# Performance work log

Hardware: AMD Instinct MI355X
Metric: run time of the kernel (lower is better)

## Reference

```python
import jax, jax.numpy as jnp
import numpy as np

SYNC = 0.15
DEBATE = 0.15
N_FACTIONS = 8


def faction_sync_debate(h, step):
    # h: [Na, H] hidden rows of alive cells (contiguous, as gathered by alive_idx)
    n, H = h.shape
    n_f = min(N_FACTIONS, n // 2)
    if n_f < 2:
        return h
    fs = n // n_f
    hb = h[: n_f * fs].reshape(n_f, fs, H)
    fm = hb.mean(axis=1, keepdims=True)                  # faction means
    hb = (1.0 - SYNC) * hb + SYNC * fm                   # sync toward faction mean
    if step > 5:                                          # step is a static Python int
        # post-sync faction means equal pre-sync means; global opinion = mean of faction means
        go = hb.mean(axis=1).mean(axis=0)                # [H]
        dc = max(1, fs // 4)
        hb = hb.at[:, :dc].set((1.0 - DEBATE) * hb[:, :dc] + DEBATE * go)
    return jnp.concatenate([hb.reshape(n_f * fs, H), h[n_f * fs:]], axis=0)


def setup_inputs() -> dict:
    key = jax.random.key(0)
    ks = jax.random.split(key, 16)
    n_cells, n_alive = 262144, 131072
    in_d, hid, out_d = 64, 128, 64
    s = 0.1
    alive_idx = jnp.sort(jax.random.permutation(ks[14], n_cells)[:n_alive])
    return {
        "x": jax.random.normal(ks[0], (1, in_d), jnp.float32),
        "hiddens": jax.random.normal(ks[1], (n_cells, hid), jnp.float32) * 0.1,
        "Wa1": jax.random.normal(ks[2], (128, in_d + hid), jnp.float32) * s,
        "ba1": jax.random.normal(ks[3], (128,), jnp.float32) * s,
        "Wa2": jax.random.normal(ks[4], (out_d, 128), jnp.float32) * s,
        "ba2": jax.random.normal(ks[5], (out_d,), jnp.float32) * s,
        "Wg1": jax.random.normal(ks[6], (128, in_d + hid), jnp.float32) * s,
        "bg1": jax.random.normal(ks[7], (128,), jnp.float32) * s,
        "Wg2": jax.random.normal(ks[8], (out_d, 128), jnp.float32) * s,
        "bg2": jax.random.normal(ks[9], (out_d,), jnp.float32) * s,
        "W_ih": jax.random.normal(ks[10], (3 * hid, out_d + 1), jnp.float32) * s,
        "W_hh": jax.random.normal(ks[11], (3 * hid, hid), jnp.float32) * s,
        "b_ih": jax.random.normal(ks[12], (3 * hid,), jnp.float32) * s,
        "b_hh": jax.random.normal(ks[13], (3 * hid,), jnp.float32) * s,
        "alive_idx": alive_idx,
        "step": 10,
    }


def reference(x, hiddens, Wa1, ba1, Wa2, ba2, Wg1, bg1, Wg2, bg2,
              W_ih, W_hh, b_ih, b_hh, alive_idx, step):
    # Gather alive cells and run the tiny MLP+GRU for all of them at once
    h = hiddens[alive_idx]                                # [Na, H]
    xb = jnp.broadcast_to(x, (h.shape[0], x.shape[-1]))   # same x for every cell
    c = jnp.concatenate([xb, h], axis=-1)                 # [Na, in+H]
    a = jax.nn.relu(c @ Wa1.T + ba1) @ Wa2.T + ba2        # engine_a
    g = jax.nn.relu(c @ Wg1.T + bg1) @ Wg2.T + bg2        # engine_g
    out = a - g                                           # [Na, D]
    tension = jnp.mean(out * out, axis=-1, keepdims=True) # [Na, 1]
    # GRUCell (torch gate order r, z, n); mem_input is detached in the original
    mem_in = jax.lax.stop_gradient(jnp.concatenate([out, tension], axis=-1))
    gi = mem_in @ W_ih.T + b_ih                           # [Na, 3H]
    gh = h @ W_hh.T + b_hh                                # [Na, 3H]
    H = h.shape[-1]
    ir, iz, inn = gi[:, :H], gi[:, H:2 * H], gi[:, 2 * H:]
    hr, hz, hn = gh[:, :H], gh[:, H:2 * H], gh[:, 2 * H:]
    r = jax.nn.sigmoid(ir + hr)
    z = jax.nn.sigmoid(iz + hz)
    nn_ = jnp.tanh(inn + r * hn)
    new_h = jax.lax.stop_gradient((1.0 - z) * nn_ + z * h)  # detached in original
    new_h = faction_sync_debate(new_h, step)
    new_hiddens = hiddens.at[alive_idx].set(new_h)        # scatter-back state update
    # tension-softmax-weighted combination (weights detached via .item() in torch)
    t = tension[:, 0]
    w = jax.lax.stop_gradient(jax.nn.softmax(t, axis=0))
    combined = jnp.sum(w[:, None] * out, axis=0, keepdims=True)  # [1, D]
    mean_tension = jnp.mean(jax.lax.stop_gradient(t))
    return combined, mean_tension, new_hiddens
```

## Files before the change

### kernel.cpp

```cpp
#include <hip/hip_runtime.h>
#include <math.h>

#define TMC 64

typedef __attribute__((ext_vector_type(4))) float f32x4;
typedef __attribute__((ext_vector_type(8))) short bf16x8;

#define MFMA16(a,b,c) __builtin_amdgcn_mfma_f32_16x16x32_bf16((a),(b),(c),0,0,0)

__device__ __forceinline__ float sigmoidf_(float x){ return 1.0f/(1.0f + __expf(-x)); }
__device__ __forceinline__ float tanhf_(float x){
  float e = __expf(2.0f*x);
  return 1.0f - 2.0f/(e + 1.0f);
}

__device__ __forceinline__ unsigned short f2bf(float f){
  unsigned u = __float_as_uint(f);
  unsigned r = (u + 0x7FFFu + ((u>>16)&1u)) >> 16;
  return (unsigned short)r;
}
__device__ __forceinline__ unsigned pack2(float a, float b){
  return (unsigned)f2bf(a) | ((unsigned)f2bf(b)<<16);
}
__device__ __forceinline__ float bf2f(unsigned short u){ return __uint_as_float(((unsigned)u)<<16); }

__device__ __forceinline__ bf16x8 lds_ld8(const ushort* base, int byte){
  return *reinterpret_cast<const bf16x8*>(reinterpret_cast<const char*>(base) + byte);
}

__global__ void k_pre(const float* __restrict__ x,
                      const float* __restrict__ Wa1, const float* __restrict__ ba1,
                      const float* __restrict__ Wg1, const float* __restrict__ bg1,
                      const float* __restrict__ ba2, const float* __restrict__ bg2,
                      const float* __restrict__ bih, const float* __restrict__ bhh,
                      float* __restrict__ xab, float* __restrict__ b2d, float* __restrict__ brz){
  __shared__ float sx[64];
  int tid = threadIdx.x;
  if (tid < 64) sx[tid] = x[tid];
  __syncthreads();
  if (tid < 128){
    const float* w = Wa1 + tid*192;
    float s = ba1[tid];
    #pragma unroll
    for (int i=0;i<64;i++) s += w[i]*sx[i];
    xab[tid] = s;
  } else {
    int j = tid-128;
    const float* w = Wg1 + j*192;
    float s = bg1[j];
    #pragma unroll
    for (int i=0;i<64;i++) s += w[i]*sx[i];
    xab[tid] = s;
  }
  if (tid < 64) b2d[tid] = ba2[tid] - bg2[tid];
  brz[tid] = bih[tid] + bhh[tid];
}

__global__ void k_pack(const float* __restrict__ Wa1, const float* __restrict__ Wg1,
                       const float* __restrict__ Wa2, const float* __restrict__ Wg2,
                       const float* __restrict__ Wih, const float* __restrict__ Whh,
                       ushort* __restrict__ W1f, ushort* __restrict__ W2f,
                       ushort* __restrict__ Wgf, ushort* __restrict__ Whf,
                       float* __restrict__ w64){
  int stride = gridDim.x*blockDim.x;
  int t0 = blockIdx.x*blockDim.x + threadIdx.x;
  for (int i=t0; i<256*128; i+=stride){
    int e=i&7, lane=(i>>3)&63, ks=(i>>9)&3, nt=i>>11;
    int r = nt*16 + (lane&15), k = ks*32 + (lane>>4)*8 + e;
    float v = (r<128) ? Wa1[r*192+64+k] : Wg1[(r-128)*192+64+k];
    W1f[i] = f2bf(v);
  }
  for (int i=t0; i<128*128; i+=stride){
    int e=i&7, lane=(i>>3)&63, ks=(i>>9)&3, nt=i>>11;
    int r = nt*16 + (lane&15), k = ks*32 + (lane>>4)*8 + e;
    float v = (r<64) ? Wa2[r*128+k] : Wg2[(r-64)*128+k];
    W2f[i] = f2bf(v);
  }
  for (int i=t0; i<384*64; i+=stride){
    int e=i&7, lane=(i>>3)&63, ks=(i>>9)&1, nt=i>>10;
    int r = nt*16 + (lane&15), k = ks*32 + (lane>>4)*8 + e;
    Wgf[i] = f2bf(Wih[r*65+k]);
  }
  for (int i=t0; i<384*128; i+=stride){
    int e=i&7, lane=(i>>3)&63, ks=(i>>9)&3, nt=i>>11;
    int r = nt*16 + (lane&15), k = ks*32 + (lane>>4)*8 + e;
    Whf[i] = f2bf(Whh[r*128+k]);
  }
  for (int i=t0; i<384; i+=stride) w64[i] = Wih[i*65+64];
}

__global__ void k_mark(const int* __restrict__ alive, int* __restrict__ iflags, int n){
  int i = blockIdx.x*blockDim.x + threadIdx.x;
  if (i < n) iflags[alive[i]] = i + 1;
}

__global__ __launch_bounds__(256,2) void k_main(
    const float* __restrict__ hiddens, const int* __restrict__ alive,
    const ushort* __restrict__ W1f, const ushort* __restrict__ W2f,
    const ushort* __restrict__ Wgf, const ushort* __restrict__ Whf,
    const float* __restrict__ w64,
    const float* __restrict__ xab, const float* __restrict__ b2d,
    const float* __restrict__ brz,
    const float* __restrict__ bih, const float* __restrict__ bhh,
    float* __restrict__ nh, float* __restrict__ facsum,
    float* __restrict__ recs, unsigned* __restrict__ tmax_u, float* __restrict__ tsum,
    int n, int fs, int nffs)
{
  __shared__ ushort sH[64*128];
  __shared__ __align__(16) ushort arena[64*256];
  __shared__ float sTS[4][64];
  __shared__ float sT[64];
  __shared__ float sE[64];
  __shared__ int   sIdx[TMC];

  ushort* sV1  = arena;
  ushort* sMIH = arena;

  int tid = threadIdx.x;
  int lane = tid & 63;
  int w = tid >> 6;
  int l15 = lane & 15;
  int lg  = lane >> 4;

  int base = blockIdx.x * TMC;
  int nvalid = n - base; if (nvalid > TMC) nvalid = TMC;

  if (tid < TMC){
    int t2 = tid < nvalid ? tid : (nvalid-1);
    sIdx[tid] = alive[base + t2];
  }
  __syncthreads();

  {
    int m = tid >> 2, c0 = (tid & 3) * 32;
    const float* src = hiddens + (size_t)sIdx[m]*128 + c0;
    #pragma unroll
    for (int j=0; j<32; j+=8){
      float4 v0 = *(const float4*)(src + j);
      float4 v1 = *(const float4*)(src + j + 4);
      uint4 pk;
      pk.x = pack2(v0.x, v0.y); pk.y = pack2(v0.z, v0.w);
      pk.z = pack2(v1.x, v1.y); pk.w = pack2(v1.z, v1.w);
      int byte = (m*256 + (c0 + j)*2) ^ ((m&7)<<4);
      *reinterpret_cast<uint4*>(reinterpret_cast<char*>(sH) + byte) = pk;
    }
  }
  __syncthreads();

  {
    int c0 = w*64;
    f32x4 acc[4][4];
    #pragma unroll
    for (int tm=0;tm<4;tm++)
      #pragma unroll
      for (int tn=0;tn<4;tn++) acc[tm][tn] = (f32x4)0.f;
    #pragma unroll
    for (int ks=0; ks<4; ks++){
      bf16x8 a[4], b[4];
      #pragma unroll
      for (int tm=0;tm<4;tm++){
        int row = tm*16 + l15;
        a[tm] = lds_ld8(sH, (row*256 + ks*64 + lg*16) ^ ((row&7)<<4));
      }
      #pragma unroll
      for (int tn=0;tn<4;tn++)
        b[tn] = *(const bf16x8*)(W1f + ((((w*4+tn)*4 + ks)*64 + lane)<<3));
      #pragma unroll
      for (int tm=0;tm<4;tm++)
        #pragma unroll
        for (int tn=0;tn<4;tn++)
          acc[tm][tn] = MFMA16(a[tm], b[tn], acc[tm][tn]);
    }
    #pragma unroll
    for (int tn=0;tn<4;tn++){
      int col = c0 + tn*16 + l15;
      float bias = xab[col];
      #pragma unroll
      for (int tm=0;tm<4;tm++){
        #pragma unroll
        for (int r=0;r<4;r++){
          int row = tm*16 + lg*4 + r;
          float v = fmaxf(acc[tm][tn][r] + bias, 0.f);
          int byte = (row*512 + col*2) ^ ((row&7)<<4);
          *(ushort*)((char*)sV1 + byte) = f2bf(v);
        }
      }
    }
  }
  __syncthreads();

  int jo2 = w*16;
  float outv[4][4];
  {
    f32x4 accA[4], accG[4];
    #pragma unroll
    for (int tm=0;tm<4;tm++){ accA[tm]=(f32x4)0.f; accG[tm]=(f32x4)0.f; }
    #pragma unroll
    for (int ks=0; ks<4; ks++){
      bf16x8 aA[4], aG[4], bA, bG;
      #pragma unroll
      for (int tm=0;tm<4;tm++){
        int row = tm*16 + l15;
        aA[tm] = lds_ld8(sV1, (row*512 + ks*64 + lg*16) ^ ((row&7)<<4));
        aG[tm] = lds_ld8(sV1, (row*512 + 256 + ks*64 + lg*16) ^ ((row&7)<<4));
      }
      bA = *(const bf16x8*)(W2f + (((w*4 + ks)*64 + lane)<<3));
      bG = *(const bf16x8*)(W2f + ((((4+w)*4 + ks)*64 + lane)<<3));
      #pragma unroll
      for (int tm=0;tm<4;tm++){
        accA[tm] = MFMA16(aA[tm], bA, accA[tm]);
        accG[tm] = MFMA16(aG[tm], bG, accG[tm]);
      }
    }
    int col = jo2 + l15;
    float bias = b2d[col];
    #pragma unroll
    for (int tm=0;tm<4;tm++)
      #pragma unroll
      for (int r=0;r<4;r++)
        outv[tm][r] = accA[tm][r] - accG[tm][r] + bias;
  }
  __syncthreads();

  {
    int col = jo2 + l15;
    float p[4][4];
    #pragma unroll
    for (int tm=0;tm<4;tm++){
      #pragma unroll
      for (int r=0;r<4;r++){
        int row = tm*16 + lg*4 + r;
        float o = outv[tm][r];
        int byte = (row*128 + col*2) ^ ((row&7)<<4);
        *(ushort*)((char*)sMIH + byte) = f2bf(o);
        p[tm][r] = o*o;
      }
    }
    #pragma unroll
    for (int off=1; off<16; off<<=1)
      #pragma unroll
      for (int tm=0;tm<4;tm++)
        #pragma unroll
        for (int r=0;r<4;r++) p[tm][r] += __shfl_xor(p[tm][r], off);
    if (l15 == 0){
      #pragma unroll
      for (int tm=0;tm<4;tm++)
        #pragma unroll
        for (int r=0;r<4;r++) sTS[w][tm*16 + lg*4 + r] = p[tm][r];
    }
  }
  __syncthreads();

  if (w == 0){
    int row = lane;
    float t = (sTS[0][row] + sTS[1][row] + sTS[2][row] + sTS[3][row]) * (1.0f/64.0f);
    sT[row] = t;
    bool valid = row < nvalid;
    float m2 = valid ? t : -1.f;
    #pragma unroll
    for (int off=1; off<64; off<<=1) m2 = fmaxf(m2, __shfl_xor(m2, off));
    float e  = valid ? __expf(t - m2) : 0.f;
    float st = valid ? t : 0.f;
    float se = e, ss = st;
    #pragma unroll
    for (int off=1; off<64; off<<=1){ se += __shfl_xor(se, off); ss += __shfl_xor(ss, off); }
    sE[row] = e;
    if (lane == 0){
      float* rec = recs + (size_t)blockIdx.x*66;
      rec[0] = m2; rec[1] = se;
      atomicMax(tmax_u, __float_as_uint(m2));
      atomicAdd(tsum, ss);
    }
  }
  __syncthreads();

  {
    float np = 0.f;
    #pragma unroll
    for (int tm=0;tm<4;tm++)
      #pragma unroll
      for (int r=0;r<4;r++)
        np += sE[tm*16 + lg*4 + r] * outv[tm][r];
    np += __shfl_xor(np, 16);
    np += __shfl_xor(np, 32);
    if (lg == 0) recs[(size_t)blockIdx.x*66 + 2 + jo2 + l15] = np;
  }

  int lastrow = nvalid;
  if (base + lastrow > nffs) lastrow = nffs - base;
  int f0 = (fs > 0 && base < nffs) ? base / fs : 0;
  bool onefac = (lastrow <= 0) || ((base + lastrow - 1) / fs == f0);

  {
    int jo3 = w*32;
    int ntb = 2*w;
    f32x4 aR[4][2], aZ[4][2], aN[4][2], aI[4][2];
    #pragma unroll
    for (int tm=0;tm<4;tm++)
      #pragma unroll
      for (int tn=0;tn<2;tn++){
        aR[tm][tn]=(f32x4)0.f; aZ[tm][tn]=(f32x4)0.f;
        aN[tm][tn]=(f32x4)0.f; aI[tm][tn]=(f32x4)0.f;
      }

    #pragma unroll
    for (int ks=0; ks<4; ks++){
      bf16x8 a[4];
      #pragma unroll
      for (int tm=0;tm<4;tm++){
        int row = tm*16 + l15;
        a[tm] = lds_ld8(sH, (row*256 + ks*64 + lg*16) ^ ((row&7)<<4));
      }
      bf16x8 bR[2], bZ[2], bN[2];
      #pragma unroll
      for (int tn=0;tn<2;tn++){
        bR[tn] = *(const bf16x8*)(Whf + ((((     ntb+tn)*4 + ks)*64 + lane)<<3));
        bZ[tn] = *(const bf16x8*)(Whf + ((((8  + ntb+tn)*4 + ks)*64 + lane)<<3));
        bN[tn] = *(const bf16x8*)(Whf + ((((16 + ntb+tn)*4 + ks)*64 + lane)<<3));
      }
      #pragma unroll
      for (int tm=0;tm<4;tm++)
        #pragma unroll
        for (int tn=0;tn<2;tn++){
          aR[tm][tn] = MFMA16(a[tm], bR[tn], aR[tm][tn]);
          aZ[tm][tn] = MFMA16(a[tm], bZ[tn], aZ[tm][tn]);
          aN[tm][tn] = MFMA16(a[tm], bN[tn], aN[tm][tn]);
        }
    }
    #pragma unroll
    for (int ks=0; ks<2; ks++){
      bf16x8 a[4];
      #pragma unroll
      for (int tm=0;tm<4;tm++){
        int row = tm*16 + l15;
        a[tm] = lds_ld8(sMIH, (row*128 + ks*64 + lg*16) ^ ((row&7)<<4));
      }
      bf16x8 bR[2], bZ[2], bI[2];
      #pragma unroll
      for (int tn=0;tn<2;tn++){
        bR[tn] = *(const bf16x8*)(Wgf + ((((     ntb+tn)*2 + ks)*64 + lane)<<3));
        bZ[tn] = *(const bf16x8*)(Wgf + ((((8  + ntb+tn)*2 + ks)*64 + lane)<<3));
        bI[tn] = *(const bf16x8*)(Wgf + ((((16 + ntb+tn)*2 + ks)*64 + lane)<<3));
      }
      #pragma unroll
      for (int tm=0;tm<4;tm++)
        #pragma unroll
        for (int tn=0;tn<2;tn++){
          aR[tm][tn] = MFMA16(a[tm], bR[tn], aR[tm][tn]);
          aZ[tm][tn] = MFMA16(a[tm], bZ[tn], aZ[tm][tn]);
          aI[tm][tn] = MFMA16(a[tm], bI[tn], aI[tm][tn]);
        }
    }

    #pragma unroll
    for (int tn=0;tn<2;tn++){
      int col = jo3 + tn*16 + l15;
      float bR0 = brz[col],      wR = w64[col];
      float bZ0 = brz[128+col],  wZ = w64[128+col];
      float bI0 = bih[256+col],  wI = w64[256+col];
      float bN0 = bhh[256+col];
      float fsum = 0.f;
      #pragma unroll
      for (int tm=0;tm<4;tm++){
        #pragma unroll
        for (int r=0;r<4;r++){
          int row = tm*16 + lg*4 + r;
          float t = sT[row];
          float rr = sigmoidf_(aR[tm][tn][r] + bR0 + t*wR);
          float zz = sigmoidf_(aZ[tm][tn][r] + bZ0 + t*wZ);
          float nnv = tanhf_(aI[tm][tn][r] + bI0 + t*wI + rr*(aN[tm][tn][r] + bN0));
          int hb = (row*256 + col*2) ^ ((row&7)<<4);
          float hv = bf2f(*(const ushort*)((const char*)sH + hb));
          float v = (1.f - zz)*nnv + zz*hv;
          if (row < nvalid) nh[(size_t)sIdx[row]*128 + col] = v;
          if (onefac){
            if (row < lastrow) fsum += v;
          } else if (row < lastrow){
            atomicAdd(&facsum[((base+row)/fs)*128 + col], v);
          }
        }
      }
      if (onefac && lastrow > 0){
        fsum += __shfl_xor(fsum, 16);
        fsum += __shfl_xor(fsum, 32);
        if (lg == 0) atomicAdd(&facsum[f0*128 + col], fsum);
      }
    }
  }
}

__global__ void k_comb1(const float* __restrict__ recs, int nrec,
                        const unsigned* __restrict__ tmax_u,
                        float* __restrict__ num, float* __restrict__ S){
  int tid = threadIdx.x;
  int c = tid & 63, rg = tid >> 6;
  float M = __uint_as_float(*tmax_u);
  float acc = 0.f, sacc = 0.f;
  for (int r = blockIdx.x*4 + rg; r < nrec; r += gridDim.x*4){
    const float* rec = recs + (size_t)r*66;
    float e = __expf(rec[0] - M);
    acc += e * rec[2+c];
    if (c == 0) sacc += e * rec[1];
  }
  __shared__ float sn[4][64];
  __shared__ float ss[4];
  sn[rg][c] = acc;
  if (c == 0) ss[rg] = sacc;
  __syncthreads();
  if (tid < 64) atomicAdd(&num[tid], sn[0][tid]+sn[1][tid]+sn[2][tid]+sn[3][tid]);
  if (tid == 64) atomicAdd(S, ss[0]+ss[1]+ss[2]+ss[3]);
}

__global__ void k_final(const float* __restrict__ num, const float* __restrict__ S,
                        const float* __restrict__ tsum, const float* __restrict__ facsum,
                        float* __restrict__ out, float* __restrict__ go, float* __restrict__ fmn,
                        int n, int n_f, int fs){
  int tid = threadIdx.x;
  if (tid < 64) out[tid] = num[tid] / *S;
  else if (tid == 64) out[64] = *tsum / (float)n;
  if (tid >= 128 && n_f >= 2){
    int j = tid - 128;
    float s = 0.f;
    for (int f=0; f<n_f; f++){
      float v = facsum[f*128+j];
      s += v;
      fmn[f*128+j] = v / (float)fs;
    }
    go[j] = s / (float)(n_f*fs);
  }
}

__global__ void k_post(const float* __restrict__ hid, const int* __restrict__ iflags,
                       const float* __restrict__ fmn, const float* __restrict__ go,
                       const int* __restrict__ step_p,
                       float* __restrict__ nh, int fs, int dc, int nffs, int total){
  bool debate = (*step_p > 5);
  int stride = gridDim.x*blockDim.x;
  for (int idx = blockIdx.x*blockDim.x + threadIdx.x; idx < total; idx += stride){
    int c = idx >> 5, q = idx & 31, j0 = q*4;
    size_t off = (size_t)c*128 + j0;
    int fl = iflags[c];
    if (fl == 0){
      float4 h4 = *(const float4*)(hid + off);
      nh[off] = h4.x; nh[off+1] = h4.y; nh[off+2] = h4.z; nh[off+3] = h4.w;
    } else {
      int i = fl - 1;
      if (i < nffs){
        float v0 = nh[off], v1 = nh[off+1], v2 = nh[off+2], v3 = nh[off+3];
        int f = i / fs;
        float4 fm4 = *(const float4*)(fmn + f*128 + j0);
        v0 = 0.85f*v0 + 0.15f*fm4.x;
        v1 = 0.85f*v1 + 0.15f*fm4.y;
        v2 = 0.85f*v2 + 0.15f*fm4.z;
        v3 = 0.85f*v3 + 0.15f*fm4.w;
        if (debate && (i - f*fs) < dc){
          float4 g4 = *(const float4*)(go + j0);
          v0 = 0.85f*v0 + 0.15f*g4.x;
          v1 = 0.85f*v1 + 0.15f*g4.y;
          v2 = 0.85f*v2 + 0.15f*g4.z;
          v3 = 0.85f*v3 + 0.15f*g4.w;
        }
        nh[off] = v0; nh[off+1] = v1; nh[off+2] = v2; nh[off+3] = v3;
      }
    }
  }
}

extern "C" void kernel_launch(void* const* d_in, const int* in_sizes, int n_in,
                              void* d_out, int out_size, void* d_ws, size_t ws_size,
                              hipStream_t stream){
  const float* x    = (const float*)d_in[0];
  const float* hid  = (const float*)d_in[1];
  const float* Wa1  = (const float*)d_in[2];
  const float* ba1  = (const float*)d_in[3];
  const float* Wa2  = (const float*)d_in[4];
  const float* ba2  = (const float*)d_in[5];
  const float* Wg1  = (const float*)d_in[6];
  const float* bg1  = (const float*)d_in[7];
  const float* Wg2  = (const float*)d_in[8];
  const float* bg2  = (const float*)d_in[9];
  const float* Wih  = (const float*)d_in[10];
  const float* Whh  = (const float*)d_in[11];
  const float* bih  = (const float*)d_in[12];
  const float* bhh  = (const float*)d_in[13];
  const int*   alive= (const int*)d_in[14];
  const int*   step = (const int*)d_in[15];

  int n = in_sizes[14];
  int n_cells = in_sizes[1] / 128;
  int n_f = (n/2 < 8) ? n/2 : 8;
  int fs   = (n_f >= 2) ? n / n_f : 0;
  int nffs = (n_f >= 2) ? n_f * fs : 0;
  int dc   = (fs/4 > 1) ? fs/4 : 1;
  int nblocks = (n + TMC - 1) / TMC;

  float* out = (float*)d_out;
  float* nh  = out + 65;
  float* ws  = (float*)d_ws;

  float* xab   = ws + 0;
  float* b2d   = ws + 256;
  float* brz   = ws + 320;
  float* facs  = ws + 576;
  float* num   = ws + 1600;
  float* Ssum  = ws + 1664;
  float* tsum  = ws + 1665;
  unsigned* tmax_u = (unsigned*)(ws + 1666);
  float* go    = ws + 1668;
  float* fmn   = ws + 1796;
  float* w64   = ws + 2820;
  float* recs  = ws + 3204;
  int recs_end = 3204 + ((nblocks*66 + 3) & ~3);
  int* iflags  = (int*)(ws + recs_end);
  int woff = (recs_end + n_cells + 3) & ~3;
  ushort* W1f  = (ushort*)(ws + woff);
  ushort* W2f  = (ushort*)(ws + woff + 16384);
  ushort* Wgf  = (ushort*)(ws + woff + 24576);
  ushort* Whf  = (ushort*)(ws + woff + 36864);

  hipMemsetAsync(ws + 576, 0, 1092*sizeof(float), stream);
  hipMemsetAsync(iflags, 0, (size_t)n_cells*sizeof(int), stream);

  k_pre<<<1,256,0,stream>>>(x, Wa1, ba1, Wg1, bg1, ba2, bg2, bih, bhh, xab, b2d, brz);
  k_pack<<<256,256,0,stream>>>(Wa1, Wg1, Wa2, Wg2, Wih, Whh, W1f, W2f, Wgf, Whf, w64);
  k_mark<<<(n+255)/256,256,0,stream>>>(alive, iflags, n);
  k_main<<<nblocks,256,0,stream>>>(hid, alive, W1f, W2f, Wgf, Whf, w64, xab, b2d, brz,
                                   bih, bhh, nh, facs, recs, tmax_u, tsum,
                                   n, fs, nffs);
  k_comb1<<<64,256,0,stream>>>(recs, nblocks, tmax_u, num, Ssum);
  k_final<<<1,256,0,stream>>>(num, Ssum, tsum, facs, out, go, fmn, n, n_f, fs);
  k_post<<<2048,256,0,stream>>>(hid, iflags, fmn, go, step, nh, fs, dc, nffs, n_cells*32);
}
```

Baseline: 183.4 us.

## Split k_main work across 8 waves with 512-thread blocks

```diff
diff --git a/kernel.cpp b/kernel.cpp
--- a/kernel.cpp
+++ b/kernel.cpp
@@ -94,7 +94,7 @@
   if (i < n) iflags[alive[i]] = i + 1;
 }
 
-__global__ __launch_bounds__(256,2) void k_main(
+__global__ __launch_bounds__(512,4) void k_main(
     const float* __restrict__ hiddens, const int* __restrict__ alive,
     const ushort* __restrict__ W1f, const ushort* __restrict__ W2f,
     const ushort* __restrict__ Wgf, const ushort* __restrict__ Whf,
@@ -108,7 +108,8 @@
 {
   __shared__ ushort sH[64*128];
   __shared__ __align__(16) ushort arena[64*256];
-  __shared__ float sTS[4][64];
+  __shared__ float sTS[8][32];
+  __shared__ float sNp[2][64];
   __shared__ float sT[64];
   __shared__ float sE[64];
   __shared__ int   sIdx[TMC];
@@ -132,10 +133,10 @@
   __syncthreads();
 
   {
-    int m = tid >> 2, c0 = (tid & 3) * 32;
+    int m = tid >> 3, c0 = (tid & 7) * 16;
     const float* src = hiddens + (size_t)sIdx[m]*128 + c0;
     #pragma unroll
-    for (int j=0; j<32; j+=8){
+    for (int j=0; j<16; j+=8){
       float4 v0 = *(const float4*)(src + j);
       float4 v1 = *(const float4*)(src + j + 4);
       uint4 pk;
@@ -148,32 +149,29 @@
   __syncthreads();
 
   {
-    int c0 = w*64;
-    f32x4 acc[4][4];
-    #pragma unroll
-    for (int tm=0;tm<4;tm++)
-      #pragma unroll
-      for (int tn=0;tn<4;tn++) acc[tm][tn] = (f32x4)0.f;
+    f32x4 acc[4][2];
+    #pragma unroll
+    for (int tm=0;tm<4;tm++){ acc[tm][0]=(f32x4)0.f; acc[tm][1]=(f32x4)0.f; }
     #pragma unroll
     for (int ks=0; ks<4; ks++){
-      bf16x8 a[4], b[4];
+      bf16x8 a[4], b[2];
       #pragma unroll
       for (int tm=0;tm<4;tm++){
         int row = tm*16 + l15;
         a[tm] = lds_ld8(sH, (row*256 + ks*64 + lg*16) ^ ((row&7)<<4));
       }
       #pragma unroll
-      for (int tn=0;tn<4;tn++)
-        b[tn] = *(const bf16x8*)(W1f + ((((w*4+tn)*4 + ks)*64 + lane)<<3));
+      for (int tn=0;tn<2;tn++)
+        b[tn] = *(const bf16x8*)(W1f + ((((w*2+tn)*4 + ks)*64 + lane)<<3));
       #pragma unroll
       for (int tm=0;tm<4;tm++)
         #pragma unroll
-        for (int tn=0;tn<4;tn++)
+        for (int tn=0;tn<2;tn++)
           acc[tm][tn] = MFMA16(a[tm], b[tn], acc[tm][tn]);
     }
     #pragma unroll
-    for (int tn=0;tn<4;tn++){
-      int col = c0 + tn*16 + l15;
+    for (int tn=0;tn<2;tn++){
+      int col = (w*2+tn)*16 + l15;
       float bias = xab[col];
       #pragma unroll
       for (int tm=0;tm<4;tm++){
@@ -189,25 +187,26 @@
   }
   __syncthreads();
 
-  int jo2 = w*16;
-  float outv[4][4];
+  int ct = w & 3, mh = w >> 2;
+  int jo2 = ct*16;
+  float outv[2][4];
   {
-    f32x4 accA[4], accG[4];
-    #pragma unroll
-    for (int tm=0;tm<4;tm++){ accA[tm]=(f32x4)0.f; accG[tm]=(f32x4)0.f; }
+    f32x4 accA[2], accG[2];
+    #pragma unroll
+    for (int tm=0;tm<2;tm++){ accA[tm]=(f32x4)0.f; accG[tm]=(f32x4)0.f; }
     #pragma unroll
     for (int ks=0; ks<4; ks++){
-      bf16x8 aA[4], aG[4], bA, bG;
-      #pragma unroll
-      for (int tm=0;tm<4;tm++){
-        int row = tm*16 + l15;
+      bf16x8 aA[2], aG[2], bA, bG;
+      #pragma unroll
+      for (int tm=0;tm<2;tm++){
+        int row = mh*32 + tm*16 + l15;
         aA[tm] = lds_ld8(sV1, (row*512 + ks*64 + lg*16) ^ ((row&7)<<4));
         aG[tm] = lds_ld8(sV1, (row*512 + 256 + ks*64 + lg*16) ^ ((row&7)<<4));
       }
-      bA = *(const bf16x8*)(W2f + (((w*4 + ks)*64 + lane)<<3));
-      bG = *(const bf16x8*)(W2f + ((((4+w)*4 + ks)*64 + lane)<<3));
-      #pragma unroll
-      for (int tm=0;tm<4;tm++){
+      bA = *(const bf16x8*)(W2f + (((ct*4 + ks)*64 + lane)<<3));
+      bG = *(const bf16x8*)(W2f + ((((4+ct)*4 + ks)*64 + lane)<<3));
+      #pragma unroll
+      for (int tm=0;tm<2;tm++){
         accA[tm] = MFMA16(aA[tm], bA, accA[tm]);
         accG[tm] = MFMA16(aG[tm], bG, accG[tm]);
       }
@@ -215,7 +214,7 @@
     int col = jo2 + l15;
     float bias = b2d[col];
     #pragma unroll
-    for (int tm=0;tm<4;tm++)
+    for (int tm=0;tm<2;tm++)
       #pragma unroll
       for (int r=0;r<4;r++)
         outv[tm][r] = accA[tm][r] - accG[tm][r] + bias;
@@ -224,12 +223,12 @@
 
   {
     int col = jo2 + l15;
-    float p[4][4];
-    #pragma unroll
-    for (int tm=0;tm<4;tm++){
+    float p[2][4];
+    #pragma unroll
+    for (int tm=0;tm<2;tm++){
       #pragma unroll
       for (int r=0;r<4;r++){
-        int row = tm*16 + lg*4 + r;
+        int row = mh*32 + tm*16 + lg*4 + r;
         float o = outv[tm][r];
         int byte = (row*128 + col*2) ^ ((row&7)<<4);
         *(ushort*)((char*)sMIH + byte) = f2bf(o);
@@ -239,12 +238,12 @@
     #pragma unroll
     for (int off=1; off<16; off<<=1)
       #pragma unroll
-      for (int tm=0;tm<4;tm++)
+      for (int tm=0;tm<2;tm++)
         #pragma unroll
         for (int r=0;r<4;r++) p[tm][r] += __shfl_xor(p[tm][r], off);
     if (l15 == 0){
       #pragma unroll
-      for (int tm=0;tm<4;tm++)
+      for (int tm=0;tm<2;tm++)
         #pragma unroll
         for (int r=0;r<4;r++) sTS[w][tm*16 + lg*4 + r] = p[tm][r];
     }
@@ -253,7 +252,8 @@
 
   if (w == 0){
     int row = lane;
-    float t = (sTS[0][row] + sTS[1][row] + sTS[2][row] + sTS[3][row]) * (1.0f/64.0f);
+    int hh = row >> 5, ri = row & 31;
+    float t = (sTS[hh*4+0][ri] + sTS[hh*4+1][ri] + sTS[hh*4+2][ri] + sTS[hh*4+3][ri]) * (1.0f/64.0f);
     sT[row] = t;
     bool valid = row < nvalid;
     float m2 = valid ? t : -1.f;
@@ -277,14 +277,16 @@
   {
     float np = 0.f;
     #pragma unroll
-    for (int tm=0;tm<4;tm++)
+    for (int tm=0;tm<2;tm++)
       #pragma unroll
       for (int r=0;r<4;r++)
-        np += sE[tm*16 + lg*4 + r] * outv[tm][r];
+        np += sE[mh*32 + tm*16 + lg*4 + r] * outv[tm][r];
     np += __shfl_xor(np, 16);
     np += __shfl_xor(np, 32);
-    if (lg == 0) recs[(size_t)blockIdx.x*66 + 2 + jo2 + l15] = np;
-  }
+    if (lg == 0) sNp[mh][jo2 + l15] = np;
+  }
+  __syncthreads();
+  if (tid < 64) recs[(size_t)blockIdx.x*66 + 2 + tid] = sNp[0][tid] + sNp[1][tid];
 
   int lastrow = nvalid;
   if (base + lastrow > nffs) lastrow = nffs - base;
@@ -292,16 +294,11 @@
   bool onefac = (lastrow <= 0) || ((base + lastrow - 1) / fs == f0);
 
   {
-    int jo3 = w*32;
-    int ntb = 2*w;
-    f32x4 aR[4][2], aZ[4][2], aN[4][2], aI[4][2];
-    #pragma unroll
-    for (int tm=0;tm<4;tm++)
-      #pragma unroll
-      for (int tn=0;tn<2;tn++){
-        aR[tm][tn]=(f32x4)0.f; aZ[tm][tn]=(f32x4)0.f;
-        aN[tm][tn]=(f32x4)0.f; aI[tm][tn]=(f32x4)0.f;
-      }
+    f32x4 aR[4], aZ[4], aN[4], aI[4];
+    #pragma unroll
+    for (int tm=0;tm<4;tm++){
+      aR[tm]=(f32x4)0.f; aZ[tm]=(f32x4)0.f; aN[tm]=(f32x4)0.f; aI[tm]=(f32x4)0.f;
+    }
 
     #pragma unroll
     for (int ks=0; ks<4; ks++){
@@ -311,21 +308,15 @@
         int row = tm*16 + l15;
         a[tm] = lds_ld8(sH, (row*256 + ks*64 + lg*16) ^ ((row&7)<<4));
       }
-      bf16x8 bR[2], bZ[2], bN[2];
-      #pragma unroll
-      for (int tn=0;tn<2;tn++){
-        bR[tn] = *(const bf16x8*)(Whf + ((((     ntb+tn)*4 + ks)*64 + lane)<<3));
-        bZ[tn] = *(const bf16x8*)(Whf + ((((8  + ntb+tn)*4 + ks)*64 + lane)<<3));
-        bN[tn] = *(const bf16x8*)(Whf + ((((16 + ntb+tn)*4 + ks)*64 + lane)<<3));
-      }
-      #pragma unroll
-      for (int tm=0;tm<4;tm++)
-        #pragma unroll
-        for (int tn=0;tn<2;tn++){
-          aR[tm][tn] = MFMA16(a[tm], bR[tn], aR[tm][tn]);
-          aZ[tm][tn] = MFMA16(a[tm], bZ[tn], aZ[tm][tn]);
-          aN[tm][tn] = MFMA16(a[tm], bN[tn], aN[tm][tn]);
-        }
+      bf16x8 bR = *(const bf16x8*)(Whf + (((      w *4 + ks)*64 + lane)<<3));
+      bf16x8 bZ = *(const bf16x8*)(Whf + ((((8  + w)*4 + ks)*64 + lane)<<3));
+      bf16x8 bN = *(const bf16x8*)(Whf + ((((16 + w)*4 + ks)*64 + lane)<<3));
+      #pragma unroll
+      for (int tm=0;tm<4;tm++){
+        aR[tm] = MFMA16(a[tm], bR, aR[tm]);
+        aZ[tm] = MFMA16(a[tm], bZ, aZ[tm]);
+        aN[tm] = MFMA16(a[tm], bN, aN[tm]);
+      }
     }
     #pragma unroll
     for (int ks=0; ks<2; ks++){
@@ -335,26 +326,19 @@
         int row = tm*16 + l15;
         a[tm] = lds_ld8(sMIH, (row*128 + ks*64 + lg*16) ^ ((row&7)<<4));
       }
-      bf16x8 bR[2], bZ[2], bI[2];
-      #pragma unroll
-      for (int tn=0;tn<2;tn++){
-        bR[tn] = *(const bf16x8*)(Wgf + ((((     ntb+tn)*2 + ks)*64 + lane)<<3));
-        bZ[tn] = *(const bf16x8*)(Wgf + ((((8  + ntb+tn)*2 + ks)*64 + lane)<<3));
-        bI[tn] = *(const bf16x8*)(Wgf + ((((16 + ntb+tn)*2 + ks)*64 + lane)<<3));
-      }
-      #pragma unroll
-      for (int tm=0;tm<4;tm++)
-        #pragma unroll
-        for (int tn=0;tn<2;tn++){
-          aR[tm][tn] = MFMA16(a[tm], bR[tn], aR[tm][tn]);
-          aZ[tm][tn] = MFMA16(a[tm], bZ[tn], aZ[tm][tn]);
-          aI[tm][tn] = MFMA16(a[tm], bI[tn], aI[tm][tn]);
-        }
-    }
-
-    #pragma unroll
-    for (int tn=0;tn<2;tn++){
-      int col = jo3 + tn*16 + l15;
+      bf16x8 bR = *(const bf16x8*)(Wgf + (((      w *2 + ks)*64 + lane)<<3));
+      bf16x8 bZ = *(const bf16x8*)(Wgf + ((((8  + w)*2 + ks)*64 + lane)<<3));
+      bf16x8 bI = *(const bf16x8*)(Wgf + ((((16 + w)*2 + ks)*64 + lane)<<3));
+      #pragma unroll
+      for (int tm=0;tm<4;tm++){
+        aR[tm] = MFMA16(a[tm], bR, aR[tm]);
+        aZ[tm] = MFMA16(a[tm], bZ, aZ[tm]);
+        aI[tm] = MFMA16(a[tm], bI, aI[tm]);
+      }
+    }
+
+    {
+      int col = w*16 + l15;
       float bR0 = brz[col],      wR = w64[col];
       float bZ0 = brz[128+col],  wZ = w64[128+col];
       float bI0 = bih[256+col],  wI = w64[256+col];
@@ -366,9 +350,9 @@
         for (int r=0;r<4;r++){
           int row = tm*16 + lg*4 + r;
           float t = sT[row];
-          float rr = sigmoidf_(aR[tm][tn][r] + bR0 + t*wR);
-          float zz = sigmoidf_(aZ[tm][tn][r] + bZ0 + t*wZ);
-          float nnv = tanhf_(aI[tm][tn][r] + bI0 + t*wI + rr*(aN[tm][tn][r] + bN0));
+          float rr = sigmoidf_(aR[tm][r] + bR0 + t*wR);
+          float zz = sigmoidf_(aZ[tm][r] + bZ0 + t*wZ);
+          float nnv = tanhf_(aI[tm][r] + bI0 + t*wI + rr*(aN[tm][r] + bN0));
           int hb = (row*256 + col*2) ^ ((row&7)<<4);
           float hv = bf2f(*(const ushort*)((const char*)sH + hb));
           float v = (1.f - zz)*nnv + zz*hv;
@@ -524,7 +508,7 @@
   k_pre<<<1,256,0,stream>>>(x, Wa1, ba1, Wg1, bg1, ba2, bg2, bih, bhh, xab, b2d, brz);
   k_pack<<<256,256,0,stream>>>(Wa1, Wg1, Wa2, Wg2, Wih, Whh, W1f, W2f, Wgf, Whf, w64);
   k_mark<<<(n+255)/256,256,0,stream>>>(alive, iflags, n);
-  k_main<<<nblocks,256,0,stream>>>(hid, alive, W1f, W2f, Wgf, Whf, w64, xab, b2d, brz,
+  k_main<<<nblocks,512,0,stream>>>(hid, alive, W1f, W2f, Wgf, Whf, w64, xab, b2d, brz,
                                    bih, bhh, nh, facs, recs, tmax_u, tsum,
                                    n, fs, nffs);
   k_comb1<<<64,256,0,stream>>>(recs, nblocks, tmax_u, num, Ssum);
```

Measured after the change: 190.8 us. 1.04x slower.
